# Kernel optimization log

Hardware: AMD Instinct MI355X
Metric: run time of the kernel (lower is better)

The kernel has to match this reference:

```python
import jax, jax.numpy as jnp
import numpy as np
import math

B, H, N, D = 4, 16, 2048, 64
SCALE = 1.0 / math.sqrt(D)

def setup_inputs() -> dict:
    key = jax.random.key(0)
    kq, kk, kv = jax.random.split(key, 3)
    return {
        "Q": jax.random.normal(kq, (B, H, N, D), dtype=jnp.float32),
        "K": jax.random.normal(kk, (B, H, N, D), dtype=jnp.float32),
        "V": jax.random.normal(kv, (B, H, N, D), dtype=jnp.float32),
    }

def reference(Q, K, V):
    # scores: [B,H,N,N] -- deliberately materialized, matching the torch module
    scores = jnp.einsum("bhnd,bhmd->bhnm", Q, K) * SCALE
    attn = jax.nn.softmax(scores, axis=-1)
    out = jnp.einsum("bhnm,bhmd->bhnd", attn, V)
    return out
```

## Files before the change

### kernel.cpp

```cpp
#include <hip/hip_runtime.h>

#define NSEQ 2048
#define DH 64
#define QSCALE (0.125f * 1.44269504088896340736f)
#define DEFER_THR 11.5415603f
#define QBLK 256
#define KVBLK 64
#define NTILE (NSEQ / KVBLK)
#define KP 72

typedef _Float16 f16x8 __attribute__((ext_vector_type(8)));
typedef _Float16 f16x4 __attribute__((ext_vector_type(4)));
typedef __fp16 fp16x2 __attribute__((ext_vector_type(2)));
typedef float f32x4 __attribute__((ext_vector_type(4)));
typedef unsigned u32x2 __attribute__((ext_vector_type(2)));

#if defined(__has_builtin) && __has_builtin(__builtin_amdgcn_exp2f)
#define EXP2R(x) __builtin_amdgcn_exp2f(x)
#else
static __device__ __forceinline__ float EXP2R(float x) {
    float r; asm("v_exp_f32 %0, %1" : "=v"(r) : "v"(x)); return r;
}
#endif

union TrP { f16x4 h[2]; f16x8 v8; };

#define TRRD(dst, bb, lit) \
    asm volatile("ds_read_b64_tr_b16 %0, %1 offset:" lit : "=v"(dst) : "v"(bb))

#define CVT4(dst, f4) do { \
        union { fp16x2 f2[2]; f16x4 h4; } _u; \
        _u.f2[0] = __builtin_amdgcn_cvt_pkrtz((f4).x, (f4).y); \
        _u.f2[1] = __builtin_amdgcn_cvt_pkrtz((f4).z, (f4).w); \
        (dst) = _u.h4; } while (0)

__global__ __launch_bounds__(512, 4)
void fa_fwd(const float* __restrict__ Qg, const float* __restrict__ Kg,
            const float* __restrict__ Vg, float* __restrict__ Og)
{
    __shared__ _Float16 Kt[2][KVBLK * KP];
    __shared__ _Float16 Vt[2][KVBLK * DH];

    const int tid  = threadIdx.x;
    const int lane = tid & 63;
    const int wv   = tid >> 6;
    const int l15  = lane & 15;
    const int g    = lane >> 4;

    const int id  = blockIdx.x;
    const int w   = (id & 7) * 64 + (id >> 3);
    const int bh  = w >> 3;
    const int qb0 = (w & 7) * QBLK;
    const size_t base = (size_t)bh * NSEQ * DH;

    f16x8 qf[2][2];
#pragma unroll
    for (int u = 0; u < 2; ++u) {
        const float* qp = Qg + base + (size_t)(qb0 + wv * 32 + u * 16 + l15) * DH;
#pragma unroll
        for (int ks = 0; ks < 2; ++ks)
#pragma unroll
            for (int j = 0; j < 8; ++j)
                qf[u][ks][j] = (_Float16)(qp[32 * ks + 8 * g + j] * QSCALE);
    }

    f32x4 acc[2][4];
#pragma unroll
    for (int u = 0; u < 2; ++u)
#pragma unroll
        for (int nt = 0; nt < 4; ++nt)
            acc[u][nt] = (f32x4){0.f, 0.f, 0.f, 0.f};
    float m_run[2] = {-INFINITY, -INFINITY};
    float l_run[2] = {0.f, 0.f};

    const int grp = tid >> 4;
    const int kb4 = grp >> 1;
    const int dh  = (grp & 1) * 32;
    const int kva = kb4 * 4 + (l15 >> 2);
    const int d0a = dh + (l15 & 3) * 4;
    const int d0b = d0a + 16;
    const float* Kbp = Kg + base;
    const float* Vbp = Vg + base;
    const int offA = kva * DH + d0a;
    const int offB = kva * DH + d0b;
    const int vta = ((kva >> 2) * 4 + (d0a >> 4)) * 64 + (kva & 3) * 16 + (d0a & 15);
    const int vtb = ((kva >> 2) * 4 + (d0b >> 4)) * 64 + (kva & 3) * 16 + (d0b & 15);
    const int kta = kva * KP + d0a;
    const int ktb = kva * KP + d0b;

    float4 kra, krb, vra, vrb;
    kra = *(const float4*)(Kbp + offA);
    krb = *(const float4*)(Kbp + offB);
    vra = *(const float4*)(Vbp + offA);
    vrb = *(const float4*)(Vbp + offB);

#define STAGE_WRITE(bb) do { \
        f16x4 h; \
        CVT4(h, kra); *(f16x4*)&Kt[bb][kta] = h; \
        CVT4(h, krb); *(f16x4*)&Kt[bb][ktb] = h; \
        CVT4(h, vra); *(f16x4*)&Vt[bb][vta] = h; \
        CVT4(h, vrb); *(f16x4*)&Vt[bb][vtb] = h; \
    } while (0)

    STAGE_WRITE(0);
    __syncthreads();

    const unsigned vtrb = (unsigned)(size_t)(&Vt[0][0]) + (unsigned)(g * 1024 + l15 * 8);

    for (int t = 0; t < NTILE; ++t) {
        const int c = t & 1;

        if (t + 1 < NTILE) {
            const float* kp = Kbp + (size_t)(t + 1) * KVBLK * DH;
            const float* vp = Vbp + (size_t)(t + 1) * KVBLK * DH;
            kra = *(const float4*)(kp + offA);
            krb = *(const float4*)(kp + offB);
            vra = *(const float4*)(vp + offA);
            vrb = *(const float4*)(vp + offB);
        }

        const unsigned vb  = vtrb + (unsigned)(c * 8192);
        const unsigned b00 = vb;
        const unsigned b01 = vb + 512u;
        const unsigned b10 = vb + 4096u;
        const unsigned b11 = vb + 4608u;

        f32x4 s[2][4];
        __builtin_amdgcn_s_setprio(1);
#pragma unroll
        for (int mt = 0; mt < 4; ++mt) {
            const f16x8 k0 = *(const f16x8*)&Kt[c][(l15 + 16 * mt) * KP + 8 * g];
            const f16x8 k1 = *(const f16x8*)&Kt[c][(l15 + 16 * mt) * KP + 32 + 8 * g];
            s[0][mt] = __builtin_amdgcn_mfma_f32_16x16x32_f16(k0, qf[0][0],
                           (f32x4){0.f, 0.f, 0.f, 0.f}, 0, 0, 0);
            s[0][mt] = __builtin_amdgcn_mfma_f32_16x16x32_f16(k1, qf[0][1], s[0][mt], 0, 0, 0);
            s[1][mt] = __builtin_amdgcn_mfma_f32_16x16x32_f16(k0, qf[1][0],
                           (f32x4){0.f, 0.f, 0.f, 0.f}, 0, 0, 0);
            s[1][mt] = __builtin_amdgcn_mfma_f32_16x16x32_f16(k1, qf[1][1], s[1][mt], 0, 0, 0);
        }
        __builtin_amdgcn_s_setprio(0);

        unsigned W[2][4][2];
#pragma unroll
        for (int u = 0; u < 2; ++u) {
            float m0 = fmaxf(fmaxf(s[u][0][0], s[u][0][1]), s[u][0][2]);
            float m1 = fmaxf(fmaxf(s[u][0][3], s[u][1][0]), s[u][1][1]);
            float m2 = fmaxf(fmaxf(s[u][1][2], s[u][1][3]), s[u][2][0]);
            float m3 = fmaxf(fmaxf(s[u][2][1], s[u][2][2]), s[u][2][3]);
            float m4 = fmaxf(fmaxf(s[u][3][0], s[u][3][1]), s[u][3][2]);
            float tmax = fmaxf(fmaxf(m0, m1), fmaxf(fmaxf(m2, m3), fmaxf(m4, s[u][3][3])));
            tmax = fmaxf(tmax, __shfl_xor(tmax, 16));
            tmax = fmaxf(tmax, __shfl_xor(tmax, 32));

            if (!__all(tmax <= m_run[u] + DEFER_THR)) {
                const float m_new = fmaxf(m_run[u], tmax);
                const float fac = EXP2R(m_run[u] - m_new);
                l_run[u] *= fac;
                m_run[u] = m_new;
#pragma unroll
                for (int r = 0; r < 4; ++r) {
                    const float fr = __shfl(fac, 4 * g + r);
#pragma unroll
                    for (int nt = 0; nt < 4; ++nt) acc[u][nt][r] *= fr;
                }
            }

            float psum = 0.f;
#pragma unroll
            for (int mt = 0; mt < 4; ++mt) {
                float p0 = EXP2R(s[u][mt][0] - m_run[u]);
                float p1 = EXP2R(s[u][mt][1] - m_run[u]);
                float p2 = EXP2R(s[u][mt][2] - m_run[u]);
                float p3 = EXP2R(s[u][mt][3] - m_run[u]);
                psum += (p0 + p1) + (p2 + p3);
                union { fp16x2 f2; unsigned w; } u0, u1;
                u0.f2 = __builtin_amdgcn_cvt_pkrtz(p0, p1);
                u1.f2 = __builtin_amdgcn_cvt_pkrtz(p2, p3);
                W[u][mt][0] = u0.w;
                W[u][mt][1] = u1.w;
            }
            psum += __shfl_xor(psum, 16);
            psum += __shfl_xor(psum, 32);
            l_run[u] += psum;
        }

#pragma unroll
        for (int ks = 0; ks < 2; ++ks) {
            TrP tp[4];
            const unsigned bh0 = ks ? b10 : b00;
            const unsigned bh1 = ks ? b11 : b01;
            TRRD(tp[0].h[0], bh0, "0");   TRRD(tp[0].h[1], bh1, "0");
            TRRD(tp[1].h[0], bh0, "128"); TRRD(tp[1].h[1], bh1, "128");
            TRRD(tp[2].h[0], bh0, "256"); TRRD(tp[2].h[1], bh1, "256");
            TRRD(tp[3].h[0], bh0, "384"); TRRD(tp[3].h[1], bh1, "384");
            asm volatile("s_waitcnt lgkmcnt(0)" ::: "memory");
            __builtin_amdgcn_sched_barrier(0);

#pragma unroll
            for (int u = 0; u < 2; ++u) {
                unsigned Ta[4];
#pragma unroll
                for (int h = 0; h < 2; ++h) {
                    u32x2 r1 = __builtin_amdgcn_permlane32_swap(W[u][2 * ks][h], W[u][2 * ks + 1][h], false, false);
                    u32x2 r2 = __builtin_amdgcn_permlane16_swap(r1[0], r1[1], false, false);
                    Ta[h]     = r2[0];
                    Ta[2 + h] = r2[1];
                }
                union { unsigned w[4]; f16x8 v; } pau;
                pau.w[0] = Ta[0]; pau.w[1] = Ta[1];
                pau.w[2] = Ta[2]; pau.w[3] = Ta[3];

                __builtin_amdgcn_s_setprio(1);
#pragma unroll
                for (int nt = 0; nt < 4; ++nt)
                    acc[u][nt] = __builtin_amdgcn_mfma_f32_16x16x32_f16(pau.v, tp[nt].v8, acc[u][nt], 0, 0, 0);
                __builtin_amdgcn_s_setprio(0);
            }
        }

        if (t + 1 < NTILE) {
            STAGE_WRITE(c ^ 1);
            __syncthreads();
        }
    }

#pragma unroll
    for (int u = 0; u < 2; ++u)
#pragma unroll
        for (int r = 0; r < 4; ++r) {
            const float lr  = __shfl(l_run[u], 4 * g + r);
            const float inv = 1.0f / lr;
            const int row = qb0 + wv * 32 + u * 16 + 4 * g + r;
            float* op = Og + base + (size_t)row * DH;
#pragma unroll
            for (int nt = 0; nt < 4; ++nt)
                op[16 * nt + l15] = acc[u][nt][r] * inv;
        }
}

extern "C" void kernel_launch(void* const* d_in, const int* in_sizes, int n_in,
                              void* d_out, int out_size, void* d_ws, size_t ws_size,
                              hipStream_t stream) {
    const float* Q = (const float*)d_in[0];
    const float* K = (const float*)d_in[1];
    const float* V = (const float*)d_in[2];
    float* O = (float*)d_out;
    fa_fwd<<<dim3(512, 1, 1), dim3(512, 1, 1), 0, stream>>>(Q, K, V, O);
}
```

Measured before the change: 101.1 us.

## Double KV tile to 128 rows and defer row-sum cross-lane reduction

Doubles the KV block staged through shared memory per iteration, processing it as two 64-row halves inside the loop, so the number of barriers and stage-write phases is halved. Each thread now prefetches four float4 of K and four of V per tile instead of two. The per-tile shuffle reduction of the softmax partial sum is moved to a single reduction after the loop, because the per-lane partials are rescaled consistently. The cost is more staging registers and double the LDS footprint, which may lower occupancy.

```diff
diff --git a/kernel.cpp b/kernel.cpp
--- a/kernel.cpp
+++ b/kernel.cpp
@@ -5,7 +5,7 @@
 #define QSCALE (0.125f * 1.44269504088896340736f)
 #define DEFER_THR 11.5415603f
 #define QBLK 256
-#define KVBLK 64
+#define KVBLK 128
 #define NTILE (NSEQ / KVBLK)
 #define KP 72
 
@@ -75,33 +75,47 @@
 
     const int grp = tid >> 4;
     const int kb4 = grp >> 1;
-    const int dh  = (grp & 1) * 32;
+    const int dhh = (grp & 1) * 32;
     const int kva = kb4 * 4 + (l15 >> 2);
-    const int d0a = dh + (l15 & 3) * 4;
+    const int d0a = dhh + (l15 & 3) * 4;
     const int d0b = d0a + 16;
     const float* Kbp = Kg + base;
     const float* Vbp = Vg + base;
     const int offA = kva * DH + d0a;
     const int offB = kva * DH + d0b;
+    const int offC = offA + 64 * DH;
+    const int offD = offB + 64 * DH;
     const int vta = ((kva >> 2) * 4 + (d0a >> 4)) * 64 + (kva & 3) * 16 + (d0a & 15);
     const int vtb = ((kva >> 2) * 4 + (d0b >> 4)) * 64 + (kva & 3) * 16 + (d0b & 15);
+    const int vtc = vta + 4096;
+    const int vtd = vtb + 4096;
     const int kta = kva * KP + d0a;
     const int ktb = kva * KP + d0b;
-
-    float4 kra, krb, vra, vrb;
-    kra = *(const float4*)(Kbp + offA);
-    krb = *(const float4*)(Kbp + offB);
-    vra = *(const float4*)(Vbp + offA);
-    vrb = *(const float4*)(Vbp + offB);
+    const int ktc = kta + 64 * KP;
+    const int ktd = ktb + 64 * KP;
+
+    float4 kra, krb, krc, krd, vra, vrb, vrc, vrd;
+#define STAGE_LOAD(p_) do { \
+        const float* kp_ = Kbp + (p_); const float* vp_ = Vbp + (p_); \
+        kra = *(const float4*)(kp_ + offA); krb = *(const float4*)(kp_ + offB); \
+        krc = *(const float4*)(kp_ + offC); krd = *(const float4*)(kp_ + offD); \
+        vra = *(const float4*)(vp_ + offA); vrb = *(const float4*)(vp_ + offB); \
+        vrc = *(const float4*)(vp_ + offC); vrd = *(const float4*)(vp_ + offD); \
+    } while (0)
 
 #define STAGE_WRITE(bb) do { \
         f16x4 h; \
         CVT4(h, kra); *(f16x4*)&Kt[bb][kta] = h; \
         CVT4(h, krb); *(f16x4*)&Kt[bb][ktb] = h; \
+        CVT4(h, krc); *(f16x4*)&Kt[bb][ktc] = h; \
+        CVT4(h, krd); *(f16x4*)&Kt[bb][ktd] = h; \
         CVT4(h, vra); *(f16x4*)&Vt[bb][vta] = h; \
         CVT4(h, vrb); *(f16x4*)&Vt[bb][vtb] = h; \
+        CVT4(h, vrc); *(f16x4*)&Vt[bb][vtc] = h; \
+        CVT4(h, vrd); *(f16x4*)&Vt[bb][vtd] = h; \
     } while (0)
 
+    STAGE_LOAD(0);
     STAGE_WRITE(0);
     __syncthreads();
 
@@ -110,111 +124,110 @@
     for (int t = 0; t < NTILE; ++t) {
         const int c = t & 1;
 
-        if (t + 1 < NTILE) {
-            const float* kp = Kbp + (size_t)(t + 1) * KVBLK * DH;
-            const float* vp = Vbp + (size_t)(t + 1) * KVBLK * DH;
-            kra = *(const float4*)(kp + offA);
-            krb = *(const float4*)(kp + offB);
-            vra = *(const float4*)(vp + offA);
-            vrb = *(const float4*)(vp + offB);
-        }
-
-        const unsigned vb  = vtrb + (unsigned)(c * 8192);
-        const unsigned b00 = vb;
-        const unsigned b01 = vb + 512u;
-        const unsigned b10 = vb + 4096u;
-        const unsigned b11 = vb + 4608u;
-
-        f32x4 s[2][4];
-        __builtin_amdgcn_s_setprio(1);
-#pragma unroll
-        for (int mt = 0; mt < 4; ++mt) {
-            const f16x8 k0 = *(const f16x8*)&Kt[c][(l15 + 16 * mt) * KP + 8 * g];
-            const f16x8 k1 = *(const f16x8*)&Kt[c][(l15 + 16 * mt) * KP + 32 + 8 * g];
-            s[0][mt] = __builtin_amdgcn_mfma_f32_16x16x32_f16(k0, qf[0][0],
-                           (f32x4){0.f, 0.f, 0.f, 0.f}, 0, 0, 0);
-            s[0][mt] = __builtin_amdgcn_mfma_f32_16x16x32_f16(k1, qf[0][1], s[0][mt], 0, 0, 0);
-            s[1][mt] = __builtin_amdgcn_mfma_f32_16x16x32_f16(k0, qf[1][0],
-                           (f32x4){0.f, 0.f, 0.f, 0.f}, 0, 0, 0);
-            s[1][mt] = __builtin_amdgcn_mfma_f32_16x16x32_f16(k1, qf[1][1], s[1][mt], 0, 0, 0);
-        }
-        __builtin_amdgcn_s_setprio(0);
-
-        unsigned W[2][4][2];
-#pragma unroll
-        for (int u = 0; u < 2; ++u) {
-            float m0 = fmaxf(fmaxf(s[u][0][0], s[u][0][1]), s[u][0][2]);
-            float m1 = fmaxf(fmaxf(s[u][0][3], s[u][1][0]), s[u][1][1]);
-            float m2 = fmaxf(fmaxf(s[u][1][2], s[u][1][3]), s[u][2][0]);
-            float m3 = fmaxf(fmaxf(s[u][2][1], s[u][2][2]), s[u][2][3]);
-            float m4 = fmaxf(fmaxf(s[u][3][0], s[u][3][1]), s[u][3][2]);
-            float tmax = fmaxf(fmaxf(m0, m1), fmaxf(fmaxf(m2, m3), fmaxf(m4, s[u][3][3])));
-            tmax = fmaxf(tmax, __shfl_xor(tmax, 16));
-            tmax = fmaxf(tmax, __shfl_xor(tmax, 32));
-
-            if (!__all(tmax <= m_run[u] + DEFER_THR)) {
-                const float m_new = fmaxf(m_run[u], tmax);
-                const float fac = EXP2R(m_run[u] - m_new);
-                l_run[u] *= fac;
-                m_run[u] = m_new;
-#pragma unroll
-                for (int r = 0; r < 4; ++r) {
-                    const float fr = __shfl(fac, 4 * g + r);
-#pragma unroll
-                    for (int nt = 0; nt < 4; ++nt) acc[u][nt][r] *= fr;
+        if (t + 1 < NTILE)
+            STAGE_LOAD((size_t)(t + 1) * KVBLK * DH);
+
+        const unsigned vbuf = vtrb + (unsigned)(c * 16384);
+
+#pragma unroll
+        for (int hf = 0; hf < 2; ++hf) {
+            const int krow0 = 64 * hf;
+            const unsigned vb0 = vbuf + (unsigned)(hf * 8192);
+            const unsigned b00 = vb0;
+            const unsigned b01 = vb0 + 512u;
+            const unsigned b10 = vb0 + 4096u;
+            const unsigned b11 = vb0 + 4608u;
+
+            f32x4 s[2][4];
+            __builtin_amdgcn_s_setprio(1);
+#pragma unroll
+            for (int mt = 0; mt < 4; ++mt) {
+                const int row = (krow0 + l15 + 16 * mt) * KP;
+                const f16x8 k0 = *(const f16x8*)&Kt[c][row + 8 * g];
+                const f16x8 k1 = *(const f16x8*)&Kt[c][row + 32 + 8 * g];
+                s[0][mt] = __builtin_amdgcn_mfma_f32_16x16x32_f16(k0, qf[0][0],
+                               (f32x4){0.f, 0.f, 0.f, 0.f}, 0, 0, 0);
+                s[0][mt] = __builtin_amdgcn_mfma_f32_16x16x32_f16(k1, qf[0][1], s[0][mt], 0, 0, 0);
+                s[1][mt] = __builtin_amdgcn_mfma_f32_16x16x32_f16(k0, qf[1][0],
+                               (f32x4){0.f, 0.f, 0.f, 0.f}, 0, 0, 0);
+                s[1][mt] = __builtin_amdgcn_mfma_f32_16x16x32_f16(k1, qf[1][1], s[1][mt], 0, 0, 0);
+            }
+            __builtin_amdgcn_s_setprio(0);
+
+            unsigned W[2][4][2];
+#pragma unroll
+            for (int u = 0; u < 2; ++u) {
+                float m0 = fmaxf(fmaxf(s[u][0][0], s[u][0][1]), s[u][0][2]);
+                float m1 = fmaxf(fmaxf(s[u][0][3], s[u][1][0]), s[u][1][1]);
+                float m2 = fmaxf(fmaxf(s[u][1][2], s[u][1][3]), s[u][2][0]);
+                float m3 = fmaxf(fmaxf(s[u][2][1], s[u][2][2]), s[u][2][3]);
+                float m4 = fmaxf(fmaxf(s[u][3][0], s[u][3][1]), s[u][3][2]);
+                float tmax = fmaxf(fmaxf(m0, m1), fmaxf(fmaxf(m2, m3), fmaxf(m4, s[u][3][3])));
+                tmax = fmaxf(tmax, __shfl_xor(tmax, 16));
+                tmax = fmaxf(tmax, __shfl_xor(tmax, 32));
+
+                if (!__all(tmax <= m_run[u] + DEFER_THR)) {
+                    const float m_new = fmaxf(m_run[u], tmax);
+                    const float fac = EXP2R(m_run[u] - m_new);
+                    l_run[u] *= fac;
+                    m_run[u] = m_new;
+#pragma unroll
+                    for (int r = 0; r < 4; ++r) {
+                        const float fr = __shfl(fac, 4 * g + r);
+#pragma unroll
+                        for (int nt = 0; nt < 4; ++nt) acc[u][nt][r] *= fr;
+                    }
                 }
+
+                float psum = 0.f;
+#pragma unroll
+                for (int mt = 0; mt < 4; ++mt) {
+                    float p0 = EXP2R(s[u][mt][0] - m_run[u]);
+                    float p1 = EXP2R(s[u][mt][1] - m_run[u]);
+                    float p2 = EXP2R(s[u][mt][2] - m_run[u]);
+                    float p3 = EXP2R(s[u][mt][3] - m_run[u]);
+                    psum += (p0 + p1) + (p2 + p3);
+                    union { fp16x2 f2; unsigned w; } u0, u1;
+                    u0.f2 = __builtin_amdgcn_cvt_pkrtz(p0, p1);
+                    u1.f2 = __builtin_amdgcn_cvt_pkrtz(p2, p3);
+                    W[u][mt][0] = u0.w;
+                    W[u][mt][1] = u1.w;
+                }
+                l_run[u] += psum;
             }
 
-            float psum = 0.f;
-#pragma unroll
-            for (int mt = 0; mt < 4; ++mt) {
-                float p0 = EXP2R(s[u][mt][0] - m_run[u]);
-                float p1 = EXP2R(s[u][mt][1] - m_run[u]);
-                float p2 = EXP2R(s[u][mt][2] - m_run[u]);
-                float p3 = EXP2R(s[u][mt][3] - m_run[u]);
-                psum += (p0 + p1) + (p2 + p3);
-                union { fp16x2 f2; unsigned w; } u0, u1;
-                u0.f2 = __builtin_amdgcn_cvt_pkrtz(p0, p1);
-                u1.f2 = __builtin_amdgcn_cvt_pkrtz(p2, p3);
-                W[u][mt][0] = u0.w;
-                W[u][mt][1] = u1.w;
-            }
-            psum += __shfl_xor(psum, 16);
-            psum += __shfl_xor(psum, 32);
-            l_run[u] += psum;
-        }
-
-#pragma unroll
-        for (int ks = 0; ks < 2; ++ks) {
-            TrP tp[4];
-            const unsigned bh0 = ks ? b10 : b00;
-            const unsigned bh1 = ks ? b11 : b01;
-            TRRD(tp[0].h[0], bh0, "0");   TRRD(tp[0].h[1], bh1, "0");
-            TRRD(tp[1].h[0], bh0, "128"); TRRD(tp[1].h[1], bh1, "128");
-            TRRD(tp[2].h[0], bh0, "256"); TRRD(tp[2].h[1], bh1, "256");
-            TRRD(tp[3].h[0], bh0, "384"); TRRD(tp[3].h[1], bh1, "384");
-            asm volatile("s_waitcnt lgkmcnt(0)" ::: "memory");
-            __builtin_amdgcn_sched_barrier(0);
-
-#pragma unroll
-            for (int u = 0; u < 2; ++u) {
-                unsigned Ta[4];
-#pragma unroll
-                for (int h = 0; h < 2; ++h) {
-                    u32x2 r1 = __builtin_amdgcn_permlane32_swap(W[u][2 * ks][h], W[u][2 * ks + 1][h], false, false);
-                    u32x2 r2 = __builtin_amdgcn_permlane16_swap(r1[0], r1[1], false, false);
-                    Ta[h]     = r2[0];
-                    Ta[2 + h] = r2[1];
+#pragma unroll
+            for (int ks = 0; ks < 2; ++ks) {
+                TrP tp[4];
+                const unsigned bh0 = ks ? b10 : b00;
+                const unsigned bh1 = ks ? b11 : b01;
+                TRRD(tp[0].h[0], bh0, "0");   TRRD(tp[0].h[1], bh1, "0");
+                TRRD(tp[1].h[0], bh0, "128"); TRRD(tp[1].h[1], bh1, "128");
+                TRRD(tp[2].h[0], bh0, "256"); TRRD(tp[2].h[1], bh1, "256");
+                TRRD(tp[3].h[0], bh0, "384"); TRRD(tp[3].h[1], bh1, "384");
+                asm volatile("s_waitcnt lgkmcnt(0)" ::: "memory");
+                __builtin_amdgcn_sched_barrier(0);
+
+#pragma unroll
+                for (int u = 0; u < 2; ++u) {
+                    unsigned Ta[4];
+#pragma unroll
+                    for (int h = 0; h < 2; ++h) {
+                        u32x2 r1 = __builtin_amdgcn_permlane32_swap(W[u][2 * ks][h], W[u][2 * ks + 1][h], false, false);
+                        u32x2 r2 = __builtin_amdgcn_permlane16_swap(r1[0], r1[1], false, false);
+                        Ta[h]     = r2[0];
+                        Ta[2 + h] = r2[1];
+                    }
+                    union { unsigned w[4]; f16x8 v; } pau;
+                    pau.w[0] = Ta[0]; pau.w[1] = Ta[1];
+                    pau.w[2] = Ta[2]; pau.w[3] = Ta[3];
+
+                    __builtin_amdgcn_s_setprio(1);
+#pragma unroll
+                    for (int nt = 0; nt < 4; ++nt)
+                        acc[u][nt] = __builtin_amdgcn_mfma_f32_16x16x32_f16(pau.v, tp[nt].v8, acc[u][nt], 0, 0, 0);
+                    __builtin_amdgcn_s_setprio(0);
                 }
-                union { unsigned w[4]; f16x8 v; } pau;
-                pau.w[0] = Ta[0]; pau.w[1] = Ta[1];
-                pau.w[2] = Ta[2]; pau.w[3] = Ta[3];
-
-                __builtin_amdgcn_s_setprio(1);
-#pragma unroll
-                for (int nt = 0; nt < 4; ++nt)
-                    acc[u][nt] = __builtin_amdgcn_mfma_f32_16x16x32_f16(pau.v, tp[nt].v8, acc[u][nt], 0, 0, 0);
-                __builtin_amdgcn_s_setprio(0);
             }
         }
 
@@ -225,7 +238,9 @@
     }
 
 #pragma unroll
-    for (int u = 0; u < 2; ++u)
+    for (int u = 0; u < 2; ++u) {
+        l_run[u] += __shfl_xor(l_run[u], 16);
+        l_run[u] += __shfl_xor(l_run[u], 32);
 #pragma unroll
         for (int r = 0; r < 4; ++r) {
             const float lr  = __shfl(l_run[u], 4 * g + r);
@@ -236,6 +251,7 @@
             for (int nt = 0; nt < 4; ++nt)
                 op[16 * nt + l15] = acc[u][nt][r] * inv;
         }
+    }
 }
 
 extern "C" void kernel_launch(void* const* d_in, const int* in_sizes, int n_in,
```

Result: slower. 175.8 us (+73.8%).
